# Kernel optimization log

Hardware: AMD Instinct MI355X
Metric: run time of the kernel (lower is better)

Reference implementation:

```python
import jax, jax.numpy as jnp
import numpy as np

ALPHA = 0.2  # LeakyReLU negative slope
EPS = 1e-8


def setup_inputs() -> dict:
    key = jax.random.key(0)
    ks = jax.random.split(key, 7)
    N, Fin, Fout, E = 100000, 256, 128, 800000
    node_embedding = jax.random.normal(ks[0], (N, Fin), dtype=jnp.float32)
    adj_pos = jax.random.randint(ks[1], (2, E), 0, N, dtype=jnp.int64)
    adj_neg = jax.random.randint(ks[2], (2, E), 0, N, dtype=jnp.int64)
    edge_embedding = jax.random.normal(ks[3], (2, Fout), dtype=jnp.float32)
    Wr = jax.random.normal(ks[4], (2, Fin, Fout), dtype=jnp.float32) * 0.05
    a = jax.random.normal(ks[5], (1, 2 * Fout), dtype=jnp.float32) * 0.05
    bias = jax.random.normal(ks[6], (1, Fout), dtype=jnp.float32) * 0.05
    return dict(node_embedding=node_embedding, edge_embedding=edge_embedding,
                Wr=Wr, a=a, bias=bias, adj_pos=adj_pos, adj_neg=adj_neg)


def reference(node_embedding, edge_embedding, Wr, a, bias, adj_pos, adj_neg):
    N = node_embedding.shape[0]
    Fout = Wr.shape[2]
    # h_r = X @ Wr[r], then column-scale by edge_embedding[r] (== mm with diag)
    h_pos = (node_embedding @ Wr[0]) * edge_embedding[0]  # [N, Fout]
    h_neg = (node_embedding @ Wr[1]) * edge_embedding[1]  # [N, Fout]
    a_src = a[0, :Fout]  # attention weights for source half of concat
    a_dst = a[0, Fout:]  # attention weights for dest half

    def edge_scores(h, adj):
        # a . [h[src], h[dst]] computed as node-level dots then scalar gather
        s = h @ a_src  # [N]
        d = h @ a_dst  # [N]
        z = s[adj[0]] + d[adj[1]]  # [E]
        z = jnp.where(z > 0, z, ALPHA * z)  # LeakyReLU
        return jax.nn.sigmoid(z)

    e_pos = edge_scores(h_pos, adj_pos)  # [E_pos]
    e_neg = edge_scores(h_neg, adj_neg)  # [E_neg]

    # row-sum normalizer: spmm(edge, edge_e, ones) == segment_sum over row idx
    rows = jnp.concatenate([adj_pos[0], adj_neg[0]])
    e_all = jnp.concatenate([e_pos, e_neg])
    row_sum = jax.ops.segment_sum(e_all, rows, num_segments=N) + EPS  # [N]

    # weighted aggregation: out[i] = sum_{(i,j)} e_ij * h[j]
    agg = (jax.ops.segment_sum(e_pos[:, None] * h_pos[adj_pos[1]], adj_pos[0], num_segments=N)
           + jax.ops.segment_sum(e_neg[:, None] * h_neg[adj_neg[1]], adj_neg[0], num_segments=N))
    return agg / row_sum[:, None] + bias
```

## Files before the change

### kernel.cpp

```cpp
#include <hip/hip_runtime.h>

#define ALPHA 0.2f
#define EPSV 1e-8f
#define BUCK_BITS 8
#define BUCK (1 << BUCK_BITS)
#define CAP 5120
#define EPB_A 4096
#define EPT_A (EPB_A / 256)
#define EQ_SCALE 16383.f

typedef float f32x4 __attribute__((ext_vector_type(4)));
typedef short bf16x8 __attribute__((ext_vector_type(8)));

static __device__ __forceinline__ unsigned short f2bf(float f) {
    union { float f; unsigned int u; } c; c.f = f;
    unsigned int u = c.u;
    unsigned int round = ((u >> 16) & 1) + 0x7FFF;
    return (unsigned short)((u + round) >> 16);
}
static __device__ __forceinline__ float bflo(unsigned int u) {
    union { unsigned int u; float f; } c; c.u = u << 16; return c.f;
}
static __device__ __forceinline__ float bfhi(unsigned int u) {
    union { unsigned int u; float f; } c; c.u = u & 0xFFFF0000u; return c.f;
}

__global__ __launch_bounds__(256) void convB_kernel(
    const float* __restrict__ Wr, uint4* __restrict__ Bp)
{
    const int t = blockIdx.x * blockDim.x + threadIdx.x;
    if (t >= 32 * 256) return;
    const int kb  = t >> 8;
    const int col = t & 255;
    const int rel = col >> 7;
    const int cc  = col & 127;
    unsigned short v[8];
    #pragma unroll
    for (int jj = 0; jj < 8; ++jj) {
        const int k = kb * 8 + jj;
        v[jj] = f2bf(Wr[(size_t)rel * 256 * 128 + (size_t)k * 128 + cc]);
    }
    Bp[t] = *reinterpret_cast<const uint4*>(v);
}

__global__ __launch_bounds__(256) void gemm_binA_kernel(
    const float* __restrict__ X, const uint4* __restrict__ Bp,
    const float* __restrict__ ee, const float* __restrict__ a,
    unsigned int* __restrict__ h32, float* __restrict__ sd,
    const int* __restrict__ adj_pos, const int* __restrict__ adj_neg,
    int* __restrict__ bucketCount, unsigned int* __restrict__ edges_tmp,
    int N, int E, int binBlocks, int totalBlocks)
{
    __shared__ char smem[16384];
    const int tid = threadIdx.x;

    const long long bi = blockIdx.x;
    const int fi  = (int)((bi * (long long)binBlocks) / totalBlocks);
    const int fi1 = (int)(((bi + 1) * (long long)binBlocks) / totalBlocks);

    if (fi1 > fi) {
        int* hist = (int*)smem;
        int* base = hist + 512;
        int* cur  = base + 512;
        const int bb = fi;
        const long long e0 = (long long)bb * EPB_A;
        const long long twoE = 2LL * E;

        hist[tid] = 0;
        hist[tid + 256] = 0;

        int esrc[EPT_A];
        unsigned int erec[EPT_A];
        #pragma unroll
        for (int k = 0; k < EPT_A; ++k) {
            const long long idx = e0 + (long long)k * 256 + tid;
            if (idx < twoE) {
                const int rel = (idx >= E) ? 1 : 0;
                const long long eidx = rel ? idx - E : idx;
                const int* __restrict__ adj = rel ? adj_neg : adj_pos;
                const int src = adj[eidx];
                const int dst = adj[E + eidx];
                esrc[k] = src;
                erec[k] = (unsigned int)dst | ((unsigned int)rel << 17) |
                          ((unsigned int)(src & (BUCK - 1)) << 18);
            } else {
                esrc[k] = -1;
            }
        }
        __syncthreads();

        #pragma unroll
        for (int k = 0; k < EPT_A; ++k)
            if (esrc[k] >= 0) atomicAdd(&hist[esrc[k] >> BUCK_BITS], 1);
        __syncthreads();

        {
            const int rot = (bb * 61) & 511;
            #pragma unroll
            for (int q = 0; q < 2; ++q) {
                const int t2 = (tid + q * 256 + rot) & 511;
                const int hv = hist[t2];
                base[t2] = hv ? atomicAdd(&bucketCount[t2], hv) : 0;
                cur[t2] = 0;
            }
        }
        __syncthreads();

        #pragma unroll
        for (int k = 0; k < EPT_A; ++k) {
            if (esrc[k] >= 0) {
                const int b = esrc[k] >> BUCK_BITS;
                const int r = atomicAdd(&cur[b], 1);
                const int pos = base[b] + r;
                if (pos < CAP)
                    edges_tmp[(size_t)b * CAP + pos] = erec[k];
            }
        }
        return;
    }

    unsigned short* Alds = (unsigned short*)smem;
    const int lane = tid & 63;
    const int w    = tid >> 6;
    const int wm   = w >> 1;
    const int wn   = w & 1;
    const int cl   = lane & 15;
    const int g    = lane >> 4;
    const int gb   = (int)bi - fi;
    const int tile0 = gb * 32;

    {
        float4 fa[4], fb[4];
        #pragma unroll
        for (int pass = 0; pass < 4; ++pass) {
            const int L  = pass * 256 + tid;
            const int r  = L >> 5;
            const int c8 = L & 31;
            const int row = tile0 + r;
            fa[pass] = make_float4(0.f, 0.f, 0.f, 0.f);
            fb[pass] = make_float4(0.f, 0.f, 0.f, 0.f);
            if (row < N) {
                const float* xp = &X[(size_t)row * 256 + c8 * 8];
                fa[pass] = *reinterpret_cast<const float4*>(xp);
                fb[pass] = *reinterpret_cast<const float4*>(xp + 4);
            }
        }
        #pragma unroll
        for (int pass = 0; pass < 4; ++pass) {
            const int L  = pass * 256 + tid;
            const int r  = L >> 5;
            const int c8 = L & 31;
            unsigned short v[8];
            v[0]=f2bf(fa[pass].x); v[1]=f2bf(fa[pass].y);
            v[2]=f2bf(fa[pass].z); v[3]=f2bf(fa[pass].w);
            v[4]=f2bf(fb[pass].x); v[5]=f2bf(fb[pass].y);
            v[6]=f2bf(fb[pass].z); v[7]=f2bf(fb[pass].w);
            const int su = c8 ^ (r & 7);
            *reinterpret_cast<bf16x8*>(&Alds[r * 256 + su * 8]) =
                *reinterpret_cast<const bf16x8*>(v);
        }
    }
    __syncthreads();

    f32x4 acc[8];
    #pragma unroll
    for (int ct = 0; ct < 8; ++ct)
        acc[ct] = (f32x4){0.f, 0.f, 0.f, 0.f};

    const int rl = wm * 16 + cl;
    #pragma unroll
    for (int kc = 0; kc < 8; ++kc) {
        const int ku = kc * 4 + g;
        const bf16x8 af = *reinterpret_cast<const bf16x8*>(
            &Alds[rl * 256 + (ku ^ (rl & 7)) * 8]);
        bf16x8 bfr[8];
        #pragma unroll
        for (int ct = 0; ct < 8; ++ct) {
            const int col = wn * 128 + ct * 16 + cl;
            bfr[ct] = *reinterpret_cast<const bf16x8*>(Bp + ku * 256 + col);
        }
        #pragma unroll
        for (int ct = 0; ct < 8; ++ct)
            acc[ct] = __builtin_amdgcn_mfma_f32_16x16x32_bf16(
                af, bfr[ct], acc[ct], 0, 0, 0);
    }

    const int rt = gb * 2 + wm;
    float eev[8], asv[8], adv[8];
    #pragma unroll
    for (int ct = 0; ct < 8; ++ct) {
        const int col = wn * 128 + ct * 16 + cl;
        const int cc  = col & 127;
        eev[ct] = ee[col];
        asv[ct] = a[cc];
        adv[ct] = a[128 + cc];
    }

    float s_acc[4], d_acc[4];
    #pragma unroll
    for (int reg = 0; reg < 4; ++reg) {
        const int row = rt * 16 + g * 4 + reg;
        const bool ok = row < N;
        float sp = 0.f, dp = 0.f;
        float vv[8];
        #pragma unroll
        for (int ct = 0; ct < 8; ++ct) {
            vv[ct] = acc[ct][reg] * eev[ct];
            sp += vv[ct] * asv[ct];
            dp += vv[ct] * adv[ct];
        }
        if (ok) {
            #pragma unroll
            for (int q = 0; q < 4; ++q) {
                const unsigned int u =
                    (unsigned int)f2bf(vv[2 * q]) |
                    ((unsigned int)f2bf(vv[2 * q + 1]) << 16);
                h32[((size_t)wn * N + row) * 64 + q * 16 + cl] = u;
            }
        }
        s_acc[reg] = sp;
        d_acc[reg] = dp;
    }
    #pragma unroll
    for (int reg = 0; reg < 4; ++reg) {
        float sp = s_acc[reg], dp = d_acc[reg];
        #pragma unroll
        for (int off = 1; off < 16; off <<= 1) {
            sp += __shfl_xor(sp, off);
            dp += __shfl_xor(dp, off);
        }
        if (cl == 0) {
            const int row = rt * 16 + g * 4 + reg;
            if (row < N) {
                sd[(size_t)wn * 2 * N + row]     = sp;
                sd[(size_t)wn * 2 * N + N + row] = dp;
            }
        }
    }
}

__global__ __launch_bounds__(512) void sortB_kernel(
    const int* __restrict__ bucketCount, const unsigned int* __restrict__ edges_tmp,
    const float* __restrict__ sd,
    unsigned int* __restrict__ edges_final,
    int* __restrict__ rowBeg, int* __restrict__ rowEnd,
    float* __restrict__ rowSum, int N)
{
    __shared__ int hist[BUCK];
    __shared__ int cur[BUCK];
    __shared__ int ssum[BUCK];
    __shared__ float sSrc[2][BUCK];
    __shared__ float rsLds[BUCK];
    const int tid = threadIdx.x;
    const int b   = blockIdx.x;
    const int s0  = b << BUCK_BITS;
    const size_t tb = (size_t)b * CAP;
    const int cnt = min(bucketCount[b], CAP);

    if (tid < BUCK) {
        hist[tid] = 0;
        rsLds[tid] = 0.f;
        const int gsrc = s0 + tid;
        sSrc[0][tid] = (gsrc < N) ? sd[gsrc] : 0.f;
        sSrc[1][tid] = (gsrc < N) ? sd[2 * (size_t)N + gsrc] : 0.f;
    }
    __syncthreads();
    for (int j = tid; j < cnt; j += 512)
        atomicAdd(&hist[edges_tmp[tb + j] >> 18], 1);
    __syncthreads();

    int h0 = 0, incl = 0;
    if (tid < BUCK) { h0 = hist[tid]; ssum[tid] = h0; incl = h0; }
    __syncthreads();
    for (int off = 1; off < BUCK; off <<= 1) {
        const int u = (tid < BUCK && tid >= off) ? ssum[tid - off] : 0;
        __syncthreads();
        if (tid < BUCK) { incl += u; ssum[tid] = incl; }
        __syncthreads();
    }
    if (tid < BUCK) {
        const int excl = incl - h0;
        cur[tid] = excl;
        const int gidx = s0 + tid;
        if (gidx < N) {
            rowBeg[gidx] = (int)tb + excl;
            rowEnd[gidx] = (int)tb + incl;
        }
    }
    __syncthreads();
    for (int j = tid; j < cnt; j += 512) {
        const unsigned int r = edges_tmp[tb + j];
        const int sl  = r >> 18;
        const int rel = (r >> 17) & 1;
        const int dst = r & 0x1FFFF;
        float z = sSrc[rel][sl] + sd[(size_t)rel * 2 * N + N + dst];
        z = z > 0.f ? z : ALPHA * z;
        const float ev = 1.f / (1.f + __expf(-z));
        const int pos = atomicAdd(&cur[sl], 1);
        atomicAdd(&rsLds[sl], ev);
        const unsigned int q = (unsigned int)(ev * EQ_SCALE + 0.5f);
        edges_final[tb + pos] = (q << 18) | (unsigned int)(rel * N + dst);
    }
    __syncthreads();
    if (tid < BUCK) {
        const int gidx = s0 + tid;
        if (gidx < N) rowSum[gidx] = rsLds[tid];
    }
}

__global__ __launch_bounds__(256) void gather_kernel(
    const int* __restrict__ rowBeg, const int* __restrict__ rowEnd,
    const float* __restrict__ rowSum,
    const unsigned int* __restrict__ edges,
    const unsigned int* __restrict__ h32,
    const float* __restrict__ bias, float* __restrict__ out, int N)
{
    const long long gw = ((long long)blockIdx.x * blockDim.x + threadIdx.x) >> 6;
    const int lane = threadIdx.x & 63;
    if (gw >= N) return;
    const int n = (int)gw;

    const int beg = rowBeg[n];
    const int end = rowEnd[n];
    const unsigned loff = (unsigned)(lane << 2);
    const char* __restrict__ hb = (const char*)h32;
    const float esc = 1.f / EQ_SCALE;

    float ax = 0.f, ay = 0.f;
    int j = beg;

    for (; j < end && (j & 3); ++j) {
        const unsigned int r = edges[j];
        const unsigned int hv = *reinterpret_cast<const unsigned int*>(
            hb + (((r & 0x3FFFFu) << 8) + loff));
        const float e = (float)(r >> 18) * esc;
        ax += e * bflo(hv);
        ay += e * bfhi(hv);
    }
    for (; j + 8 <= end; j += 8) {
        const uint4 qa = *reinterpret_cast<const uint4*>(&edges[j]);
        const uint4 qb = *reinterpret_cast<const uint4*>(&edges[j + 4]);
        const unsigned int rr[8] = {qa.x, qa.y, qa.z, qa.w,
                                    qb.x, qb.y, qb.z, qb.w};
        unsigned int hv[8];
        #pragma unroll
        for (int k = 0; k < 8; ++k)
            hv[k] = *reinterpret_cast<const unsigned int*>(
                hb + (((rr[k] & 0x3FFFFu) << 8) + loff));
        #pragma unroll
        for (int k = 0; k < 8; ++k) {
            const float e = (float)(rr[k] >> 18) * esc;
            ax += e * bflo(hv[k]);
            ay += e * bfhi(hv[k]);
        }
    }
    for (; j + 4 <= end; j += 4) {
        const uint4 qa = *reinterpret_cast<const uint4*>(&edges[j]);
        const unsigned int rr[4] = {qa.x, qa.y, qa.z, qa.w};
        unsigned int hv[4];
        #pragma unroll
        for (int k = 0; k < 4; ++k)
            hv[k] = *reinterpret_cast<const unsigned int*>(
                hb + (((rr[k] & 0x3FFFFu) << 8) + loff));
        #pragma unroll
        for (int k = 0; k < 4; ++k) {
            const float e = (float)(rr[k] >> 18) * esc;
            ax += e * bflo(hv[k]);
            ay += e * bfhi(hv[k]);
        }
    }
    for (; j < end; ++j) {
        const unsigned int r = edges[j];
        const unsigned int hv = *reinterpret_cast<const unsigned int*>(
            hb + (((r & 0x3FFFFu) << 8) + loff));
        const float e = (float)(r >> 18) * esc;
        ax += e * bflo(hv);
        ay += e * bfhi(hv);
    }
    const float inv = 1.f / (rowSum[n] + EPSV);
    const int q  = lane >> 4;
    const int cl = lane & 15;
    const int c0 = q * 32 + cl;
    const int c1 = c0 + 16;
    out[(size_t)n * 128 + c0] = ax * inv + bias[c0];
    out[(size_t)n * 128 + c1] = ay * inv + bias[c1];
}

extern "C" void kernel_launch(void* const* d_in, const int* in_sizes, int n_in,
                              void* d_out, int out_size, void* d_ws, size_t ws_size,
                              hipStream_t stream) {
    const float* X      = (const float*)d_in[0];
    const float* ee     = (const float*)d_in[1];
    const float* Wr     = (const float*)d_in[2];
    const float* a      = (const float*)d_in[3];
    const float* bias   = (const float*)d_in[4];
    const int* adj_pos  = (const int*)d_in[5];
    const int* adj_neg  = (const int*)d_in[6];

    const int N = in_sizes[0] / 256;
    const int E = in_sizes[5] / 2;
    const int twoE = 2 * E;
    float* out = (float*)d_out;

    const int gemmBlocks = (N + 31) / 32;
    const int NBUCK = (N + BUCK - 1) >> BUCK_BITS;
    const int binBlocks = (twoE + EPB_A - 1) / EPB_A;
    const int totalBlocks = binBlocks + gemmBlocks;

    char* ws = (char*)d_ws;
    uint4* Bp = (uint4*)ws;
    char* p = ws + 32 * 256 * 16;
    unsigned int* h32 = (unsigned int*)p; p += (size_t)2 * N * 64 * 4;
    float* sd         = (float*)p;  p += (size_t)4 * N * 4;
    int* bucketCount  = (int*)p;    p += 512 * 4;
    int* rowBeg       = (int*)p;    p += (size_t)N * 4;
    int* rowEnd       = (int*)p;    p += (size_t)N * 4;
    float* rowSum     = (float*)p;  p += (size_t)N * 4;
    p = (char*)(((uintptr_t)p + 15) & ~(uintptr_t)15);
    unsigned int* edges_tmp = (unsigned int*)p; p += (size_t)NBUCK * CAP * 4;
    p = (char*)(((uintptr_t)p + 15) & ~(uintptr_t)15);
    unsigned int* edges_final = (unsigned int*)p; p += (size_t)NBUCK * CAP * 4;

    (void)hipMemsetAsync(bucketCount, 0, 512 * sizeof(int), stream);

    convB_kernel<<<32, 256, 0, stream>>>(Wr, Bp);

    gemm_binA_kernel<<<totalBlocks, 256, 0, stream>>>(
        X, Bp, ee, a, h32, sd, adj_pos, adj_neg, bucketCount, edges_tmp,
        N, E, binBlocks, totalBlocks);

    sortB_kernel<<<NBUCK, 512, 0, stream>>>(
        bucketCount, edges_tmp, sd, edges_final, rowBeg, rowEnd, rowSum, N);

    gather_kernel<<<(int)(((long long)N * 64 + 255) / 256), 256, 0, stream>>>(
        rowBeg, rowEnd, rowSum, edges_final, h32, bias, out, N);
}
```

Baseline: 157.8 us.

## Fuse bucket sort and gather into one kernel with LDS-resident CSR

Merges the per-bucket counting sort and the row gather into one kernel. Each block takes a quarter of a bucket (64 source rows), sorts that slice's edges into shared memory, and then has its four waves aggregate 16 rows each straight from that LDS CSR. This removes the global edges_final, rowBeg, rowEnd and rowSum round trips and one launch. The cost is that each block rescans the whole bucket's edge list, which is four times the edge reads. Parallelism also drops to one wave per 16 rows processed one after another, and any slice with more than 1280 edges would silently drop the extras.

Result: faster. 150.8 us (-4.4%).

```diff
diff --git a/kernel.cpp b/kernel.cpp
--- a/kernel.cpp
+++ b/kernel.cpp
@@ -8,6 +8,8 @@
 #define EPB_A 4096
 #define EPT_A (EPB_A / 256)
 #define EQ_SCALE 16383.f
+#define SG_SRCS 64
+#define SG_CAP 1280
 
 typedef float f32x4 __attribute__((ext_vector_type(4)));
 typedef short bf16x8 __attribute__((ext_vector_type(8)));
@@ -239,151 +241,117 @@
     }
 }
 
-__global__ __launch_bounds__(512) void sortB_kernel(
+__global__ __launch_bounds__(256) void sort_gather_kernel(
     const int* __restrict__ bucketCount, const unsigned int* __restrict__ edges_tmp,
-    const float* __restrict__ sd,
-    unsigned int* __restrict__ edges_final,
-    int* __restrict__ rowBeg, int* __restrict__ rowEnd,
-    float* __restrict__ rowSum, int N)
-{
-    __shared__ int hist[BUCK];
-    __shared__ int cur[BUCK];
-    __shared__ int ssum[BUCK];
-    __shared__ float sSrc[2][BUCK];
-    __shared__ float rsLds[BUCK];
-    const int tid = threadIdx.x;
-    const int b   = blockIdx.x;
-    const int s0  = b << BUCK_BITS;
-    const size_t tb = (size_t)b * CAP;
-    const int cnt = min(bucketCount[b], CAP);
-
-    if (tid < BUCK) {
-        hist[tid] = 0;
-        rsLds[tid] = 0.f;
-        const int gsrc = s0 + tid;
-        sSrc[0][tid] = (gsrc < N) ? sd[gsrc] : 0.f;
-        sSrc[1][tid] = (gsrc < N) ? sd[2 * (size_t)N + gsrc] : 0.f;
-    }
-    __syncthreads();
-    for (int j = tid; j < cnt; j += 512)
-        atomicAdd(&hist[edges_tmp[tb + j] >> 18], 1);
-    __syncthreads();
-
-    int h0 = 0, incl = 0;
-    if (tid < BUCK) { h0 = hist[tid]; ssum[tid] = h0; incl = h0; }
-    __syncthreads();
-    for (int off = 1; off < BUCK; off <<= 1) {
-        const int u = (tid < BUCK && tid >= off) ? ssum[tid - off] : 0;
-        __syncthreads();
-        if (tid < BUCK) { incl += u; ssum[tid] = incl; }
-        __syncthreads();
-    }
-    if (tid < BUCK) {
-        const int excl = incl - h0;
-        cur[tid] = excl;
-        const int gidx = s0 + tid;
-        if (gidx < N) {
-            rowBeg[gidx] = (int)tb + excl;
-            rowEnd[gidx] = (int)tb + incl;
-        }
-    }
-    __syncthreads();
-    for (int j = tid; j < cnt; j += 512) {
-        const unsigned int r = edges_tmp[tb + j];
-        const int sl  = r >> 18;
-        const int rel = (r >> 17) & 1;
-        const int dst = r & 0x1FFFF;
-        float z = sSrc[rel][sl] + sd[(size_t)rel * 2 * N + N + dst];
-        z = z > 0.f ? z : ALPHA * z;
-        const float ev = 1.f / (1.f + __expf(-z));
-        const int pos = atomicAdd(&cur[sl], 1);
-        atomicAdd(&rsLds[sl], ev);
-        const unsigned int q = (unsigned int)(ev * EQ_SCALE + 0.5f);
-        edges_final[tb + pos] = (q << 18) | (unsigned int)(rel * N + dst);
-    }
-    __syncthreads();
-    if (tid < BUCK) {
-        const int gidx = s0 + tid;
-        if (gidx < N) rowSum[gidx] = rsLds[tid];
-    }
-}
-
-__global__ __launch_bounds__(256) void gather_kernel(
-    const int* __restrict__ rowBeg, const int* __restrict__ rowEnd,
-    const float* __restrict__ rowSum,
-    const unsigned int* __restrict__ edges,
-    const unsigned int* __restrict__ h32,
+    const float* __restrict__ sd, const unsigned int* __restrict__ h32,
     const float* __restrict__ bias, float* __restrict__ out, int N)
 {
-    const long long gw = ((long long)blockIdx.x * blockDim.x + threadIdx.x) >> 6;
-    const int lane = threadIdx.x & 63;
-    if (gw >= N) return;
-    const int n = (int)gw;
-
-    const int beg = rowBeg[n];
-    const int end = rowEnd[n];
+    __shared__ unsigned int csr[SG_CAP];
+    __shared__ int hist[SG_SRCS];
+    __shared__ int begs[SG_SRCS];
+    __shared__ int cur[SG_SRCS];
+    __shared__ float rsL[SG_SRCS];
+    __shared__ float sS[2][SG_SRCS];
+    const int tid  = threadIdx.x;
+    const int blk  = blockIdx.x;
+    const int b    = blk >> 2;
+    const int sbase = (blk & 3) * SG_SRCS;
+    const int s0   = (b << BUCK_BITS) + sbase;
+    const size_t tb = (size_t)b * CAP;
+    const int cnt  = min(bucketCount[b], CAP);
+
+    if (tid < SG_SRCS) {
+        hist[tid] = 0;
+        rsL[tid]  = 0.f;
+        const int gsrc = s0 + tid;
+        sS[0][tid] = (gsrc < N) ? sd[gsrc] : 0.f;
+        sS[1][tid] = (gsrc < N) ? sd[2 * (size_t)N + gsrc] : 0.f;
+    }
+    __syncthreads();
+
+    for (int j = tid; j < cnt; j += 256) {
+        const int sl = (int)(edges_tmp[tb + j] >> 18) - sbase;
+        if ((unsigned)sl < SG_SRCS) atomicAdd(&hist[sl], 1);
+    }
+    __syncthreads();
+
+    int h0 = 0, incl = 0;
+    if (tid < SG_SRCS) { h0 = hist[tid]; begs[tid] = h0; incl = h0; }
+    __syncthreads();
+    for (int off = 1; off < SG_SRCS; off <<= 1) {
+        const int u = (tid < SG_SRCS && tid >= off) ? begs[tid - off] : 0;
+        __syncthreads();
+        if (tid < SG_SRCS) { incl += u; begs[tid] = incl; }
+        __syncthreads();
+    }
+    if (tid < SG_SRCS) cur[tid] = incl - h0;
+    __syncthreads();
+    if (tid < SG_SRCS) begs[tid] = cur[tid];
+    __syncthreads();
+
+    for (int j = tid; j < cnt; j += 256) {
+        const unsigned int r = edges_tmp[tb + j];
+        const int sl = (int)(r >> 18) - sbase;
+        if ((unsigned)sl < SG_SRCS) {
+            const int rel = (r >> 17) & 1;
+            const int dst = r & 0x1FFFF;
+            float z = sS[rel][sl] + sd[(size_t)rel * 2 * N + N + dst];
+            z = z > 0.f ? z : ALPHA * z;
+            const float ev = 1.f / (1.f + __expf(-z));
+            const int pos = atomicAdd(&cur[sl], 1);
+            atomicAdd(&rsL[sl], ev);
+            const unsigned int q = (unsigned int)(ev * EQ_SCALE + 0.5f);
+            if (pos < SG_CAP)
+                csr[pos] = (q << 18) | (unsigned int)(rel * N + dst);
+        }
+    }
+    __syncthreads();
+
+    const int lane = tid & 63;
+    const int w    = tid >> 6;
     const unsigned loff = (unsigned)(lane << 2);
     const char* __restrict__ hb = (const char*)h32;
     const float esc = 1.f / EQ_SCALE;
 
-    float ax = 0.f, ay = 0.f;
-    int j = beg;
-
-    for (; j < end && (j & 3); ++j) {
-        const unsigned int r = edges[j];
-        const unsigned int hv = *reinterpret_cast<const unsigned int*>(
-            hb + (((r & 0x3FFFFu) << 8) + loff));
-        const float e = (float)(r >> 18) * esc;
-        ax += e * bflo(hv);
-        ay += e * bfhi(hv);
-    }
-    for (; j + 8 <= end; j += 8) {
-        const uint4 qa = *reinterpret_cast<const uint4*>(&edges[j]);
-        const uint4 qb = *reinterpret_cast<const uint4*>(&edges[j + 4]);
-        const unsigned int rr[8] = {qa.x, qa.y, qa.z, qa.w,
-                                    qb.x, qb.y, qb.z, qb.w};
-        unsigned int hv[8];
-        #pragma unroll
-        for (int k = 0; k < 8; ++k)
-            hv[k] = *reinterpret_cast<const unsigned int*>(
-                hb + (((rr[k] & 0x3FFFFu) << 8) + loff));
-        #pragma unroll
-        for (int k = 0; k < 8; ++k) {
-            const float e = (float)(rr[k] >> 18) * esc;
-            ax += e * bflo(hv[k]);
-            ay += e * bfhi(hv[k]);
-        }
-    }
-    for (; j + 4 <= end; j += 4) {
-        const uint4 qa = *reinterpret_cast<const uint4*>(&edges[j]);
-        const unsigned int rr[4] = {qa.x, qa.y, qa.z, qa.w};
-        unsigned int hv[4];
-        #pragma unroll
-        for (int k = 0; k < 4; ++k)
-            hv[k] = *reinterpret_cast<const unsigned int*>(
-                hb + (((rr[k] & 0x3FFFFu) << 8) + loff));
-        #pragma unroll
-        for (int k = 0; k < 4; ++k) {
-            const float e = (float)(rr[k] >> 18) * esc;
-            ax += e * bflo(hv[k]);
-            ay += e * bfhi(hv[k]);
-        }
-    }
-    for (; j < end; ++j) {
-        const unsigned int r = edges[j];
-        const unsigned int hv = *reinterpret_cast<const unsigned int*>(
-            hb + (((r & 0x3FFFFu) << 8) + loff));
-        const float e = (float)(r >> 18) * esc;
-        ax += e * bflo(hv);
-        ay += e * bfhi(hv);
-    }
-    const float inv = 1.f / (rowSum[n] + EPSV);
-    const int q  = lane >> 4;
-    const int cl = lane & 15;
-    const int c0 = q * 32 + cl;
-    const int c1 = c0 + 16;
-    out[(size_t)n * 128 + c0] = ax * inv + bias[c0];
-    out[(size_t)n * 128 + c1] = ay * inv + bias[c1];
+    for (int s = w * 16; s < w * 16 + 16; ++s) {
+        const int gsrc = s0 + s;
+        if (gsrc >= N) break;
+        const int beg = begs[s];
+        const int end = beg + hist[s];
+        float ax = 0.f, ay = 0.f;
+        int j = beg;
+        for (; j + 4 <= end; j += 4) {
+            unsigned int rr[4];
+            #pragma unroll
+            for (int k = 0; k < 4; ++k) rr[k] = csr[j + k];
+            unsigned int hv[4];
+            #pragma unroll
+            for (int k = 0; k < 4; ++k)
+                hv[k] = *reinterpret_cast<const unsigned int*>(
+                    hb + (((rr[k] & 0x3FFFFu) << 8) + loff));
+            #pragma unroll
+            for (int k = 0; k < 4; ++k) {
+                const float e = (float)(rr[k] >> 18) * esc;
+                ax += e * bflo(hv[k]);
+                ay += e * bfhi(hv[k]);
+            }
+        }
+        for (; j < end; ++j) {
+            const unsigned int r = csr[j];
+            const unsigned int hv = *reinterpret_cast<const unsigned int*>(
+                hb + (((r & 0x3FFFFu) << 8) + loff));
+            const float e = (float)(r >> 18) * esc;
+            ax += e * bflo(hv);
+            ay += e * bfhi(hv);
+        }
+        const float inv = 1.f / (rsL[s] + EPSV);
+        const int qq = lane >> 4;
+        const int cl = lane & 15;
+        const int c0 = qq * 32 + cl;
+        const int c1 = c0 + 16;
+        out[(size_t)gsrc * 128 + c0] = ax * inv + bias[c0];
+        out[(size_t)gsrc * 128 + c1] = ay * inv + bias[c1];
+    }
 }
 
 extern "C" void kernel_launch(void* const* d_in, const int* in_sizes, int n_in,
@@ -413,13 +381,8 @@
     unsigned int* h32 = (unsigned int*)p; p += (size_t)2 * N * 64 * 4;
     float* sd         = (float*)p;  p += (size_t)4 * N * 4;
     int* bucketCount  = (int*)p;    p += 512 * 4;
-    int* rowBeg       = (int*)p;    p += (size_t)N * 4;
-    int* rowEnd       = (int*)p;    p += (size_t)N * 4;
-    float* rowSum     = (float*)p;  p += (size_t)N * 4;
     p = (char*)(((uintptr_t)p + 15) & ~(uintptr_t)15);
     unsigned int* edges_tmp = (unsigned int*)p; p += (size_t)NBUCK * CAP * 4;
-    p = (char*)(((uintptr_t)p + 15) & ~(uintptr_t)15);
-    unsigned int* edges_final = (unsigned int*)p; p += (size_t)NBUCK * CAP * 4;
 
     (void)hipMemsetAsync(bucketCount, 0, 512 * sizeof(int), stream);
 
@@ -429,9 +392,6 @@
         X, Bp, ee, a, h32, sd, adj_pos, adj_neg, bucketCount, edges_tmp,
         N, E, binBlocks, totalBlocks);
 
-    sortB_kernel<<<NBUCK, 512, 0, stream>>>(
-        bucketCount, edges_tmp, sd, edges_final, rowBeg, rowEnd, rowSum, N);
-
-    gather_kernel<<<(int)(((long long)N * 64 + 255) / 256), 256, 0, stream>>>(
-        rowBeg, rowEnd, rowSum, edges_final, h32, bias, out, N);
-}
+    sort_gather_kernel<<<NBUCK * 4, 256, 0, stream>>>(
+        bucketCount, edges_tmp, sd, h32, bias, out, N);
+}
```
